# Performance work log

Measured on AMD Instinct MI355X. Metric: run time of the kernel, lower is better.

Reference implementation:

```python
import jax, jax.numpy as jnp
import numpy as np

EPS = 1e-5
DN = ('NCHW', 'OIHW', 'NCHW')


def conv3x3(x, w, b):
    y = jax.lax.conv_general_dilated(x, w, window_strides=(1, 1), padding='SAME',
                                     dimension_numbers=DN)
    return y + b[None, :, None, None]


def bn_relu(x, g, be, m, v):
    # inference-mode BatchNorm2d followed by ReLU, folded into one FMA
    inv = g / jnp.sqrt(v + EPS)
    return jax.nn.relu(x * inv[None, :, None, None] + (be - m * inv)[None, :, None, None])


def haar_idwt2(cA, cH, cV, cD):
    # pywt.idwt2(coeffs, 'db1'): cH = detail along rows (axis -2), cV = detail along cols (axis -1)
    # Exact Haar synthesis -> 2x2 pixel blocks (pixel-shuffle style, no CPU round-trip)
    p00 = (cA + cH + cV + cD) * 0.5  # (2i,   2j)
    p01 = (cA + cH - cV - cD) * 0.5  # (2i,   2j+1)
    p10 = (cA - cH + cV - cD) * 0.5  # (2i+1, 2j)
    p11 = (cA - cH - cV + cD) * 0.5  # (2i+1, 2j+1)
    B, C, H, W = cA.shape
    even = jnp.stack([p00, p01], axis=-1).reshape(B, C, H, 2 * W)
    odd = jnp.stack([p10, p11], axis=-1).reshape(B, C, H, 2 * W)
    return jnp.stack([even, odd], axis=-2).reshape(B, C, 2 * H, 2 * W)


def setup_inputs() -> dict:
    key = jax.random.key(0)
    ks = jax.random.split(key, 24)
    B, IN_C, OUT_C, H, W = 16, 128, 64, 64, 64
    d = {}
    d['x'] = jax.random.normal(ks[0], (B, IN_C, H, W), jnp.float32)
    d['s'] = jax.random.normal(ks[1], (B, OUT_C, 2 * H, 2 * W), jnp.float32)
    # input_convdwt: Conv(in_c -> 4*in_c) + BN
    d['w1'] = jax.random.normal(ks[2], (4 * IN_C, IN_C, 3, 3), jnp.float32) * 0.05
    d['b1'] = jax.random.normal(ks[3], (4 * IN_C,), jnp.float32) * 0.05
    d['g1'] = jax.random.uniform(ks[4], (4 * IN_C,), jnp.float32, 0.5, 1.5)
    d['be1'] = jax.random.normal(ks[5], (4 * IN_C,), jnp.float32) * 0.05
    d['m1'] = jax.random.normal(ks[6], (4 * IN_C,), jnp.float32) * 0.05
    d['v1'] = jax.random.uniform(ks[7], (4 * IN_C,), jnp.float32, 0.5, 1.5)
    # s_con: Conv(in_c -> out_c) + BN
    d['ws'] = jax.random.normal(ks[8], (OUT_C, IN_C, 3, 3), jnp.float32) * 0.05
    d['bs'] = jax.random.normal(ks[9], (OUT_C,), jnp.float32) * 0.05
    d['gs'] = jax.random.uniform(ks[10], (OUT_C,), jnp.float32, 0.5, 1.5)
    d['bes'] = jax.random.normal(ks[11], (OUT_C,), jnp.float32) * 0.05
    d['ms'] = jax.random.normal(ks[12], (OUT_C,), jnp.float32) * 0.05
    d['vs'] = jax.random.uniform(ks[13], (OUT_C,), jnp.float32, 0.5, 1.5)
    # conv: Conv(in_c -> out_c) + BN (applied to concat(s, s_out))
    d['w2'] = jax.random.normal(ks[14], (OUT_C, IN_C, 3, 3), jnp.float32) * 0.05
    d['b2'] = jax.random.normal(ks[15], (OUT_C,), jnp.float32) * 0.05
    d['g2'] = jax.random.uniform(ks[16], (OUT_C,), jnp.float32, 0.5, 1.5)
    d['be2'] = jax.random.normal(ks[17], (OUT_C,), jnp.float32) * 0.05
    d['m2'] = jax.random.normal(ks[18], (OUT_C,), jnp.float32) * 0.05
    d['v2'] = jax.random.uniform(ks[19], (OUT_C,), jnp.float32, 0.5, 1.5)
    return d


def reference(x, s, w1, b1, g1, be1, m1, v1,
              ws, bs, gs, bes, ms, vs,
              w2, b2, g2, be2, m2, v2):
    # input_convdwt: conv -> BN -> ReLU, channels in_c -> 4*in_c
    h = bn_relu(conv3x3(x, w1, b1), g1, be1, m1, v1)
    c = h.shape[1]
    q = c // 4
    cA, cH, cV, cD = h[:, :q], h[:, q:2 * q], h[:, 2 * q:3 * q], h[:, 3 * q:]
    idwt_out = haar_idwt2(cA, cH, cV, cD)  # (B, in_c, 2H, 2W)
    # skip-connection branch (s is not None)
    s_out = bn_relu(conv3x3(idwt_out, ws, bs), gs, bes, ms, vs)  # (B, out_c, 2H, 2W)
    concat = jnp.concatenate([s, s_out], axis=1)                  # (B, in_c, 2H, 2W)
    decoder_output = bn_relu(conv3x3(concat, w2, b2), g2, be2, m2, v2)
    return decoder_output
```

## Files before the change

kernel.cpp:

```cpp
#include <hip/hip_runtime.h>
#include <hip/hip_bf16.h>

typedef __attribute__((ext_vector_type(8))) short short8;
typedef __attribute__((ext_vector_type(4))) float f32x4;
typedef unsigned short u16;

#define EPSV 1e-5f

__device__ __forceinline__ u16 f2bf(float f) {
    __hip_bfloat16 h = __float2bfloat16(f);
    return *reinterpret_cast<u16*>(&h);
}

__global__ void cvt_kernel(const float* __restrict__ src, u16* __restrict__ dst,
                           int C, int H, int W, int units) {
    int u = blockIdx.x * 256 + threadIdx.x;
    if (u >= units) return;
    int kb = u & 3;
    int p  = u >> 2;
    int x  = p % W;  p /= W;
    int y  = p % H;  p /= H;
    int n  = p & 15;
    int cc = p >> 4;
    short8 v;
#pragma unroll
    for (int j = 0; j < 8; ++j)
        v[j] = (short)f2bf(src[(((size_t)n * C + cc * 32 + kb * 8 + j) * H + y) * W + x]);
    *(short8*)(dst + ((((size_t)cc * 16 + n) * H + y) * W + x) * 32 + kb * 8) = v;
}

__global__ void repack_w1_kernel(const float* __restrict__ w1, u16* __restrict__ wf) {
    int u = blockIdx.x * 256 + threadIdx.x;
    if (u >= 4 * 8 * 9 * 4 * 64) return;
    int l = u & 63;
    int r = u >> 6;
    int ciC = r & 3;  r >>= 2;
    int t   = r % 9;  r /= 9;
    int bt  = r & 7;
    int cc  = r >> 3;
    int co  = (bt >> 1) * 128 + cc * 32 + (bt & 1) * 16 + (l & 15);
    int ci0 = ciC * 32 + (l >> 4) * 8;
    short8 v;
#pragma unroll
    for (int e = 0; e < 8; ++e)
        v[e] = (short)f2bf(w1[((size_t)co * 128 + ci0 + e) * 9 + t]);
    *(short8*)(wf + (size_t)u * 8) = v;
}

__global__ void repack_wg_kernel(const float* __restrict__ w, u16* __restrict__ wf) {
    int u = blockIdx.x * 256 + threadIdx.x;
    if (u >= 4 * 9 * 4 * 64) return;
    int l = u & 63;
    int r = u >> 6;
    int ciC = r & 3;  r >>= 2;
    int t   = r % 9;
    int bt  = r / 9;
    int co  = bt * 16 + (l & 15);
    int ci0 = ciC * 32 + (l >> 4) * 8;
    short8 v;
#pragma unroll
    for (int e = 0; e < 8; ++e)
        v[e] = (short)f2bf(w[((size_t)co * 128 + ci0 + e) * 9 + t]);
    *(short8*)(wf + (size_t)u * 8) = v;
}

__global__ __launch_bounds__(256, 2)
void conv1_mfma_kernel(const u16* __restrict__ inb, const u16* __restrict__ wf,
                       const float* __restrict__ bb, const float* __restrict__ gg,
                       const float* __restrict__ bee, const float* __restrict__ mm,
                       const float* __restrict__ vv, u16* __restrict__ ob) {
    const int tile = blockIdx.x;
    const int cc   = blockIdx.y;
    const int n    = blockIdx.z;
    const int x0   = (tile & 3) * 16;
    const int y0   = (tile >> 2) * 8;
    const int tid  = threadIdx.x;
    const int lane = tid & 63;
    const int wid  = tid >> 6;
    const int wm   = wid >> 1;
    const int wc   = wid & 1;
    const int kb   = lane >> 4;
    const int xl   = lane & 15;

    __shared__ float4 lds4[720];
    const short8* ldsr = (const short8*)lds4;

    f32x4 acc[4][4];
#pragma unroll
    for (int j = 0; j < 4; ++j)
#pragma unroll
        for (int q = 0; q < 4; ++q) acc[j][q] = (f32x4){0.f, 0.f, 0.f, 0.f};

    float4 sreg[3];
    auto load_stage = [&](int ciC) {
#pragma unroll
        for (int p = 0; p < 3; ++p) {
            int e = p * 256 + tid;
            float4 v = make_float4(0.f, 0.f, 0.f, 0.f);
            if (e < 720) {
                int pix = e >> 2, ke = e & 3;
                int yy = pix / 18;
                int xx = pix - yy * 18;
                int gy = y0 - 1 + yy, gx = x0 - 1 + xx;
                if ((unsigned)gy < 64u && (unsigned)gx < 64u)
                    v = *(const float4*)(inb + ((((size_t)ciC * 16 + n) * 64 + gy) * 64 + gx) * 32 + ke * 8);
            }
            sreg[p] = v;
        }
    };
    auto write_stage = [&]() {
#pragma unroll
        for (int p = 0; p < 3; ++p) {
            int e = p * 256 + tid;
            if (e < 720) lds4[e ^ ((e >> 2) & 7)] = sreg[p];
        }
    };

    load_stage(0);
    for (int ciC = 0; ciC < 4; ++ciC) {
        write_stage();
        __syncthreads();
        if (ciC < 3) load_stage(ciC + 1);
#pragma unroll
        for (int t = 0; t < 9; ++t) {
            const int dy = t / 3, dx = t - (t / 3) * 3;
            short8 a[4], b[4];
#pragma unroll
            for (int j = 0; j < 4; ++j) {
                int pix = (wm * 4 + j + dy) * 18 + xl + dx;
                int e = pix * 4 + kb;
                a[j] = ldsr[e ^ ((e >> 2) & 7)];
            }
#pragma unroll
            for (int q = 0; q < 4; ++q) {
                int bt = q * 2 + wc;
                b[q] = *(const short8*)(wf + ((size_t)(((cc * 8 + bt) * 9 + t) * 4 + ciC) * 64 + lane) * 8);
            }
#pragma unroll
            for (int j = 0; j < 4; ++j)
#pragma unroll
                for (int q = 0; q < 4; ++q)
                    acc[j][q] = __builtin_amdgcn_mfma_f32_16x16x32_bf16(a[j], b[q], acc[j][q], 0, 0, 0);
        }
        __syncthreads();
    }

    float invq[4], shq[4];
#pragma unroll
    for (int q = 0; q < 4; ++q) {
        int co  = q * 128 + cc * 32 + wc * 16 + xl;
        float inv = gg[co] / sqrtf(vv[co] + EPSV);
        invq[q] = inv;
        shq[q]  = bb[co] * inv + bee[co] - mm[co] * inv;
    }
    const int c32 = wc * 16 + xl;
#pragma unroll
    for (int j = 0; j < 4; ++j) {
        int y = y0 + wm * 4 + j;
#pragma unroll
        for (int i = 0; i < 4; ++i) {
            float A_ = fmaxf(acc[j][0][i] * invq[0] + shq[0], 0.f);
            float H_ = fmaxf(acc[j][1][i] * invq[1] + shq[1], 0.f);
            float V_ = fmaxf(acc[j][2][i] * invq[2] + shq[2], 0.f);
            float D_ = fmaxf(acc[j][3][i] * invq[3] + shq[3], 0.f);
            float p00 = (A_ + H_ + V_ + D_) * 0.5f;
            float p01 = (A_ + H_ - V_ - D_) * 0.5f;
            float p10 = (A_ - H_ + V_ - D_) * 0.5f;
            float p11 = (A_ - H_ - V_ + D_) * 0.5f;
            int oy = 2 * y, ox = 2 * (x0 + kb * 4 + i);
            size_t base = ((((size_t)cc * 16 + n) * 128 + oy) * 128 + ox) * 32 + c32;
            ob[base]            = f2bf(p00);
            ob[base + 32]       = f2bf(p01);
            ob[base + 128 * 32] = f2bf(p10);
            ob[base + 128 * 32 + 32] = f2bf(p11);
        }
    }
}

template <bool FP32OUT>
__global__ __launch_bounds__(256, 2)
void convg_mfma_kernel(const u16* __restrict__ inb, const u16* __restrict__ wf,
                       const float* __restrict__ bb, const float* __restrict__ gg,
                       const float* __restrict__ bee, const float* __restrict__ mm,
                       const float* __restrict__ vv, u16* __restrict__ ob,
                       float* __restrict__ of) {
    const int tile = blockIdx.x;
    const int n    = blockIdx.y;
    const int x0   = (tile & 7) * 16;
    const int y0   = (tile >> 3) * 8;
    const int tid  = threadIdx.x;
    const int lane = tid & 63;
    const int wid  = tid >> 6;
    const int wm   = wid >> 1;
    const int wc   = wid & 1;
    const int kb   = lane >> 4;
    const int xl   = lane & 15;

    __shared__ float4 lds4[720];
    const short8* ldsr = (const short8*)lds4;

    f32x4 acc[4][2];
#pragma unroll
    for (int j = 0; j < 4; ++j)
#pragma unroll
        for (int cb = 0; cb < 2; ++cb) acc[j][cb] = (f32x4){0.f, 0.f, 0.f, 0.f};

    float4 sreg[3];
    auto load_stage = [&](int ciC) {
#pragma unroll
        for (int p = 0; p < 3; ++p) {
            int e = p * 256 + tid;
            float4 v = make_float4(0.f, 0.f, 0.f, 0.f);
            if (e < 720) {
                int pix = e >> 2, ke = e & 3;
                int yy = pix / 18;
                int xx = pix - yy * 18;
                int gy = y0 - 1 + yy, gx = x0 - 1 + xx;
                if ((unsigned)gy < 128u && (unsigned)gx < 128u)
                    v = *(const float4*)(inb + ((((size_t)ciC * 16 + n) * 128 + gy) * 128 + gx) * 32 + ke * 8);
            }
            sreg[p] = v;
        }
    };
    auto write_stage = [&]() {
#pragma unroll
        for (int p = 0; p < 3; ++p) {
            int e = p * 256 + tid;
            if (e < 720) lds4[e ^ ((e >> 2) & 7)] = sreg[p];
        }
    };

    load_stage(0);
    for (int ciC = 0; ciC < 4; ++ciC) {
        write_stage();
        __syncthreads();
        if (ciC < 3) load_stage(ciC + 1);
#pragma unroll
        for (int t = 0; t < 9; ++t) {
            const int dy = t / 3, dx = t - (t / 3) * 3;
            short8 a[4], b[2];
#pragma unroll
            for (int j = 0; j < 4; ++j) {
                int pix = (wm * 4 + j + dy) * 18 + xl + dx;
                int e = pix * 4 + kb;
                a[j] = ldsr[e ^ ((e >> 2) & 7)];
            }
#pragma unroll
            for (int cb = 0; cb < 2; ++cb) {
                int bt = wc * 2 + cb;
                b[cb] = *(const short8*)(wf + ((size_t)((bt * 9 + t) * 4 + ciC) * 64 + lane) * 8);
            }
#pragma unroll
            for (int j = 0; j < 4; ++j)
#pragma unroll
                for (int cb = 0; cb < 2; ++cb)
                    acc[j][cb] = __builtin_amdgcn_mfma_f32_16x16x32_bf16(a[j], b[cb], acc[j][cb], 0, 0, 0);
        }
        __syncthreads();
    }

#pragma unroll
    for (int cb = 0; cb < 2; ++cb) {
        int co = (wc * 2 + cb) * 16 + xl;
        float inv = gg[co] / sqrtf(vv[co] + EPSV);
        float sh  = bb[co] * inv + bee[co] - mm[co] * inv;
#pragma unroll
        for (int j = 0; j < 4; ++j) {
            int y = y0 + wm * 4 + j;
#pragma unroll
            for (int i = 0; i < 4; ++i) {
                float val = fmaxf(acc[j][cb][i] * inv + sh, 0.f);
                int xg = x0 + kb * 4 + i;
                if (FP32OUT) {
                    of[(((size_t)n * 64 + co) * 128 + y) * 128 + xg] = val;
                } else {
                    ob[((((size_t)(co >> 5) * 16 + n) * 128 + y) * 128 + xg) * 32 + (co & 31)] = f2bf(val);
                }
            }
        }
    }
}

extern "C" void kernel_launch(void* const* d_in, const int* in_sizes, int n_in,
                              void* d_out, int out_size, void* d_ws, size_t ws_size,
                              hipStream_t stream) {
    const float* x   = (const float*)d_in[0];
    const float* s   = (const float*)d_in[1];
    const float* w1  = (const float*)d_in[2];
    const float* b1  = (const float*)d_in[3];
    const float* g1  = (const float*)d_in[4];
    const float* be1 = (const float*)d_in[5];
    const float* m1  = (const float*)d_in[6];
    const float* v1  = (const float*)d_in[7];
    const float* wsw = (const float*)d_in[8];
    const float* bs  = (const float*)d_in[9];
    const float* gs  = (const float*)d_in[10];
    const float* bes = (const float*)d_in[11];
    const float* ms  = (const float*)d_in[12];
    const float* vs  = (const float*)d_in[13];
    const float* w2  = (const float*)d_in[14];
    const float* b2  = (const float*)d_in[15];
    const float* g2  = (const float*)d_in[16];
    const float* be2 = (const float*)d_in[17];
    const float* m2  = (const float*)d_in[18];
    const float* v2  = (const float*)d_in[19];
    float* out = (float*)d_out;

    char* wsp = (char*)d_ws;
    u16* xb   = (u16*)(wsp);
    u16* idwt = (u16*)(wsp + 16777216);
    u16* cat  = (u16*)(wsp + 16777216 + 67108864);
    u16* wf1  = (u16*)(wsp + 16777216 + 67108864 + 67108864);
    u16* wfS  = (u16*)(wsp + 16777216 + 67108864 + 67108864 + 1179648);
    u16* wf2  = (u16*)(wsp + 16777216 + 67108864 + 67108864 + 1179648 + 147456);

    cvt_kernel<<<dim3(4096), dim3(256), 0, stream>>>(x, xb, 128, 64, 64, 1048576);
    cvt_kernel<<<dim3(8192), dim3(256), 0, stream>>>(s, cat, 64, 128, 128, 2097152);
    repack_w1_kernel<<<dim3(288), dim3(256), 0, stream>>>(w1, wf1);
    repack_wg_kernel<<<dim3(36), dim3(256), 0, stream>>>(wsw, wfS);
    repack_wg_kernel<<<dim3(36), dim3(256), 0, stream>>>(w2, wf2);

    conv1_mfma_kernel<<<dim3(32, 4, 16), dim3(256), 0, stream>>>(
        xb, wf1, b1, g1, be1, m1, v1, idwt);

    convg_mfma_kernel<false><<<dim3(128, 16), dim3(256), 0, stream>>>(
        idwt, wfS, bs, gs, bes, ms, vs, cat + (size_t)2 * 16 * 128 * 128 * 32, nullptr);

    convg_mfma_kernel<true><<<dim3(128, 16), dim3(256), 0, stream>>>(
        cat, wf2, b2, g2, be2, m2, v2, nullptr, out);
}
```

Before: 232.7 us.

## Reuse A fragments across dy taps and enlarge convg output tile

After: 360.6 us. 1.55x slower.

```diff
diff --git a/kernel.cpp b/kernel.cpp
--- a/kernel.cpp
+++ b/kernel.cpp
@@ -64,7 +64,7 @@
     *(short8*)(wf + (size_t)u * 8) = v;
 }
 
-__global__ __launch_bounds__(256, 2)
+__global__ __launch_bounds__(256, 3)
 void conv1_mfma_kernel(const u16* __restrict__ inb, const u16* __restrict__ wf,
                        const float* __restrict__ bb, const float* __restrict__ gg,
                        const float* __restrict__ bee, const float* __restrict__ mm,
@@ -122,25 +122,29 @@
         __syncthreads();
         if (ciC < 3) load_stage(ciC + 1);
 #pragma unroll
-        for (int t = 0; t < 9; ++t) {
-            const int dy = t / 3, dx = t - (t / 3) * 3;
-            short8 a[4], b[4];
-#pragma unroll
-            for (int j = 0; j < 4; ++j) {
-                int pix = (wm * 4 + j + dy) * 18 + xl + dx;
+        for (int dx = 0; dx < 3; ++dx) {
+            short8 a[6];
+#pragma unroll
+            for (int r = 0; r < 6; ++r) {
+                int pix = (wm * 4 + r) * 18 + xl + dx;
                 int e = pix * 4 + kb;
-                a[j] = ldsr[e ^ ((e >> 2) & 7)];
-            }
-#pragma unroll
-            for (int q = 0; q < 4; ++q) {
-                int bt = q * 2 + wc;
-                b[q] = *(const short8*)(wf + ((size_t)(((cc * 8 + bt) * 9 + t) * 4 + ciC) * 64 + lane) * 8);
-            }
-#pragma unroll
-            for (int j = 0; j < 4; ++j)
-#pragma unroll
-                for (int q = 0; q < 4; ++q)
-                    acc[j][q] = __builtin_amdgcn_mfma_f32_16x16x32_bf16(a[j], b[q], acc[j][q], 0, 0, 0);
+                a[r] = ldsr[e ^ ((e >> 2) & 7)];
+            }
+#pragma unroll
+            for (int dy = 0; dy < 3; ++dy) {
+                const int t = dy * 3 + dx;
+                short8 b[4];
+#pragma unroll
+                for (int q = 0; q < 4; ++q) {
+                    int bt = q * 2 + wc;
+                    b[q] = *(const short8*)(wf + ((size_t)(((cc * 8 + bt) * 9 + t) * 4 + ciC) * 64 + lane) * 8);
+                }
+#pragma unroll
+                for (int j = 0; j < 4; ++j)
+#pragma unroll
+                    for (int q = 0; q < 4; ++q)
+                        acc[j][q] = __builtin_amdgcn_mfma_f32_16x16x32_bf16(a[j + dy], b[q], acc[j][q], 0, 0, 0);
+            }
         }
         __syncthreads();
     }
@@ -178,7 +182,7 @@
 }
 
 template <bool FP32OUT>
-__global__ __launch_bounds__(256, 2)
+__global__ __launch_bounds__(256, 3)
 void convg_mfma_kernel(const u16* __restrict__ inb, const u16* __restrict__ wf,
                        const float* __restrict__ bb, const float* __restrict__ gg,
                        const float* __restrict__ bee, const float* __restrict__ mm,
@@ -187,31 +191,29 @@
     const int tile = blockIdx.x;
     const int n    = blockIdx.y;
     const int x0   = (tile & 7) * 16;
-    const int y0   = (tile >> 3) * 8;
+    const int y0   = (tile >> 3) * 16;
     const int tid  = threadIdx.x;
     const int lane = tid & 63;
     const int wid  = tid >> 6;
-    const int wm   = wid >> 1;
-    const int wc   = wid & 1;
     const int kb   = lane >> 4;
     const int xl   = lane & 15;
 
-    __shared__ float4 lds4[720];
+    __shared__ float4 lds4[1296];
     const short8* ldsr = (const short8*)lds4;
 
-    f32x4 acc[4][2];
+    f32x4 acc[4][4];
 #pragma unroll
     for (int j = 0; j < 4; ++j)
 #pragma unroll
-        for (int cb = 0; cb < 2; ++cb) acc[j][cb] = (f32x4){0.f, 0.f, 0.f, 0.f};
-
-    float4 sreg[3];
+        for (int cb = 0; cb < 4; ++cb) acc[j][cb] = (f32x4){0.f, 0.f, 0.f, 0.f};
+
+    float4 sreg[6];
     auto load_stage = [&](int ciC) {
 #pragma unroll
-        for (int p = 0; p < 3; ++p) {
+        for (int p = 0; p < 6; ++p) {
             int e = p * 256 + tid;
             float4 v = make_float4(0.f, 0.f, 0.f, 0.f);
-            if (e < 720) {
+            if (e < 1296) {
                 int pix = e >> 2, ke = e & 3;
                 int yy = pix / 18;
                 int xx = pix - yy * 18;
@@ -224,9 +226,9 @@
     };
     auto write_stage = [&]() {
 #pragma unroll
-        for (int p = 0; p < 3; ++p) {
+        for (int p = 0; p < 6; ++p) {
             int e = p * 256 + tid;
-            if (e < 720) lds4[e ^ ((e >> 2) & 7)] = sreg[p];
+            if (e < 1296) lds4[e ^ ((e >> 2) & 7)] = sreg[p];
         }
     };
 
@@ -236,44 +238,51 @@
         __syncthreads();
         if (ciC < 3) load_stage(ciC + 1);
 #pragma unroll
-        for (int t = 0; t < 9; ++t) {
-            const int dy = t / 3, dx = t - (t / 3) * 3;
-            short8 a[4], b[2];
-#pragma unroll
-            for (int j = 0; j < 4; ++j) {
-                int pix = (wm * 4 + j + dy) * 18 + xl + dx;
+        for (int dx = 0; dx < 3; ++dx) {
+            short8 a[6];
+#pragma unroll
+            for (int r = 0; r < 6; ++r) {
+                int pix = (wid * 4 + r) * 18 + xl + dx;
                 int e = pix * 4 + kb;
-                a[j] = ldsr[e ^ ((e >> 2) & 7)];
-            }
-#pragma unroll
-            for (int cb = 0; cb < 2; ++cb) {
-                int bt = wc * 2 + cb;
-                b[cb] = *(const short8*)(wf + ((size_t)((bt * 9 + t) * 4 + ciC) * 64 + lane) * 8);
-            }
-#pragma unroll
-            for (int j = 0; j < 4; ++j)
-#pragma unroll
-                for (int cb = 0; cb < 2; ++cb)
-                    acc[j][cb] = __builtin_amdgcn_mfma_f32_16x16x32_bf16(a[j], b[cb], acc[j][cb], 0, 0, 0);
+                a[r] = ldsr[e ^ ((e >> 2) & 7)];
+            }
+#pragma unroll
+            for (int dy = 0; dy < 3; ++dy) {
+                const int t = dy * 3 + dx;
+                short8 b[4];
+#pragma unroll
+                for (int cb = 0; cb < 4; ++cb)
+                    b[cb] = *(const short8*)(wf + ((size_t)((cb * 9 + t) * 4 + ciC) * 64 + lane) * 8);
+#pragma unroll
+                for (int j = 0; j < 4; ++j)
+#pragma unroll
+                    for (int cb = 0; cb < 4; ++cb)
+                        acc[j][cb] = __builtin_amdgcn_mfma_f32_16x16x32_bf16(a[j + dy], b[cb], acc[j][cb], 0, 0, 0);
+            }
         }
         __syncthreads();
     }
 
 #pragma unroll
-    for (int cb = 0; cb < 2; ++cb) {
-        int co = (wc * 2 + cb) * 16 + xl;
+    for (int cb = 0; cb < 4; ++cb) {
+        int co = cb * 16 + xl;
         float inv = gg[co] / sqrtf(vv[co] + EPSV);
         float sh  = bb[co] * inv + bee[co] - mm[co] * inv;
 #pragma unroll
         for (int j = 0; j < 4; ++j) {
-            int y = y0 + wm * 4 + j;
-#pragma unroll
-            for (int i = 0; i < 4; ++i) {
-                float val = fmaxf(acc[j][cb][i] * inv + sh, 0.f);
-                int xg = x0 + kb * 4 + i;
-                if (FP32OUT) {
-                    of[(((size_t)n * 64 + co) * 128 + y) * 128 + xg] = val;
-                } else {
+            int y = y0 + wid * 4 + j;
+            if (FP32OUT) {
+                float4 v4;
+                v4.x = fmaxf(acc[j][cb][0] * inv + sh, 0.f);
+                v4.y = fmaxf(acc[j][cb][1] * inv + sh, 0.f);
+                v4.z = fmaxf(acc[j][cb][2] * inv + sh, 0.f);
+                v4.w = fmaxf(acc[j][cb][3] * inv + sh, 0.f);
+                *(float4*)&of[(((size_t)n * 64 + co) * 128 + y) * 128 + x0 + kb * 4] = v4;
+            } else {
+#pragma unroll
+                for (int i = 0; i < 4; ++i) {
+                    float val = fmaxf(acc[j][cb][i] * inv + sh, 0.f);
+                    int xg = x0 + kb * 4 + i;
                     ob[((((size_t)(co >> 5) * 16 + n) * 128 + y) * 128 + xg) * 32 + (co & 31)] = f2bf(val);
                 }
             }
@@ -323,9 +332,9 @@
     conv1_mfma_kernel<<<dim3(32, 4, 16), dim3(256), 0, stream>>>(
         xb, wf1, b1, g1, be1, m1, v1, idwt);
 
-    convg_mfma_kernel<false><<<dim3(128, 16), dim3(256), 0, stream>>>(
+    convg_mfma_kernel<false><<<dim3(64, 16), dim3(256), 0, stream>>>(
         idwt, wfS, bs, gs, bes, ms, vs, cat + (size_t)2 * 16 * 128 * 128 * 32, nullptr);
 
-    convg_mfma_kernel<true><<<dim3(128, 16), dim3(256), 0, stream>>>(
+    convg_mfma_kernel<true><<<dim3(64, 16), dim3(256), 0, stream>>>(
         cat, wf2, b2, g2, be2, m2, v2, nullptr, out);
 }
```
